# Kernel optimization log

Measured on AMD Instinct MI355X. Metric: run time of the kernel, lower is better.

Reference implementation:

```python
import jax, jax.numpy as jnp
import numpy as np

HEADS = 8
DIM_HEAD = 64
SCALE = DIM_HEAD ** -0.5


def setup_inputs() -> dict:
    key = jax.random.key(0)
    k1, k2, k3, k4 = jax.random.split(key, 4)
    b, dim, l = 4, 512, 2048
    hidden = HEADS * DIM_HEAD  # 512
    x = jax.random.normal(k1, (b, dim, l), dtype=jnp.float32)
    w_qkv = jax.random.normal(k2, (3 * hidden, dim), dtype=jnp.float32) * (dim ** -0.5)
    w_out = jax.random.normal(k3, (dim, hidden), dtype=jnp.float32) * (hidden ** -0.5)
    b_out = jax.random.normal(k4, (dim,), dtype=jnp.float32) * 0.01
    return {"x": x, "w_qkv": w_qkv, "w_out": w_out, "b_out": b_out}


def reference(x, w_qkv, w_out, b_out):
    b, c, l = x.shape
    h, d = HEADS, DIM_HEAD
    # 1x1 Conv1d == channel matmul: [3*hidden, c] x [b, c, l] -> [b, 3*hidden, l]
    qkv = jnp.einsum('oc,bcl->bol', w_qkv, x)
    q, k, v = jnp.split(qkv, 3, axis=1)
    # 'b (h d) l -> b h d l'
    q = q.reshape(b, h, d, l) * SCALE
    k = k.reshape(b, h, d, l)
    v = v.reshape(b, h, d, l)
    sim = jnp.einsum('bhdi,bhdj->bhij', q, k)          # [b, h, l, l]
    attn = jax.nn.softmax(sim, axis=-1)
    out = jnp.einsum('bhij,bhdj->bhid', attn, v)       # [b, h, l, d]
    # 'b h l d -> b (h d) l'
    out = out.transpose(0, 1, 3, 2).reshape(b, h * d, l)
    return jnp.einsum('oc,bcl->bol', w_out, out) + b_out[None, :, None]
```

## Files before the change

### kernel.cpp

```cpp
#include <hip/hip_runtime.h>

#define L_SEQ 2048
#define KDIM  512

typedef __attribute__((ext_vector_type(8))) short short8v;
typedef __attribute__((ext_vector_type(4))) float f32x4;

static __device__ __forceinline__ short f2b(float f) {
    union { float f; unsigned u; } v; v.f = f;
    unsigned r = v.u + 0x7fffu + ((v.u >> 16) & 1u);
    return (short)(r >> 16);
}

static __device__ __forceinline__ float fast_exp2(float x) {
#if __has_builtin(__builtin_amdgcn_exp2f)
    return __builtin_amdgcn_exp2f(x);
#else
    return exp2f(x);
#endif
}

__global__ __launch_bounds__(256) void conv_w(
    const float* __restrict__ wq, const float* __restrict__ wo,
    short* __restrict__ wqb, short* __restrict__ wob)
{
    const int i = blockIdx.x * 256 + threadIdx.x;
    const int NQ = 1536 * 512 / 4;
    float4 v;
    if (i < NQ) v = ((const float4*)wq)[i];
    else        v = ((const float4*)wo)[i - NQ];
    short4 s;
    s.x = f2b(v.x); s.y = f2b(v.y); s.z = f2b(v.z); s.w = f2b(v.w);
    if (i < NQ) ((short4*)wqb)[i] = s;
    else        ((short4*)wob)[i - NQ] = s;
}

__global__ __launch_bounds__(256) void transpose_x(
    const float* __restrict__ x, short* __restrict__ xT)
{
    const int b  = blockIdx.z;
    const int c0 = blockIdx.y * 64;
    const int l0 = blockIdx.x * 64;
    __shared__ __align__(16) float T[64 * 72];
    const int t = threadIdx.x;

#pragma unroll
    for (int j = 0; j < 4; ++j) {
        const int idx = j * 256 + t;
        const int row = idx >> 4, c4 = idx & 15;
        const float4 v = *(const float4*)&x[((size_t)b * KDIM + c0 + row) * L_SEQ + l0 + c4 * 4];
        *(float4*)&T[row * 72 + c4 * 4] = v;
    }
    __syncthreads();

#pragma unroll
    for (int j = 0; j < 2; ++j) {
        const int idx = j * 256 + t;
        const int l = idx >> 3, ch = idx & 7;
        short8v s;
#pragma unroll
        for (int e = 0; e < 8; ++e)
            s[e] = f2b(T[(ch * 8 + e) * 72 + l]);
        *(short8v*)&xT[((size_t)b * L_SEQ + l0 + l) * KDIM + c0 + ch * 8] = s;
    }
}

template<int EPI>
__global__ __launch_bounds__(256) void gemm_bt(
    const short* __restrict__ Ag, const short* __restrict__ Bbase,
    const float* __restrict__ bias,
    short* __restrict__ Qws, short* __restrict__ Kws, short* __restrict__ Vws,
    float* __restrict__ Cout)
{
    const int bz = blockIdx.z;
    const int o0 = blockIdx.y * 128;
    const int l0 = blockIdx.x * 128;
    const short* Bg = Bbase + (size_t)bz * L_SEQ * KDIM;

    __shared__ __align__(16) char smem[2 * 128 * 72 * 2];
    short* sA = (short*)smem;
    short* sB = (short*)(smem + 128 * 72 * 2);

    const int t    = threadIdx.x;
    const int w    = t >> 6;
    const int lane = t & 63;
    const int quad = lane >> 4;
    const int l16  = lane & 15;
    const int wo   = (w & 1) * 64;
    const int wl   = (w >> 1) * 64;

    f32x4 acc[4][4];
#pragma unroll
    for (int i = 0; i < 4; ++i)
#pragma unroll
        for (int n = 0; n < 4; ++n) acc[i][n] = (f32x4){0,0,0,0};

    for (int k0 = 0; k0 < KDIM; k0 += 64) {
#pragma unroll
        for (int j = 0; j < 4; ++j) {
            const int idx = j * 256 + t;
            const int r = idx >> 3, c = idx & 7;
            *(float4*)&sA[r * 72 + c * 8] =
                *(const float4*)&Ag[(size_t)(o0 + r) * KDIM + k0 + c * 8];
            *(float4*)&sB[r * 72 + c * 8] =
                *(const float4*)&Bg[(size_t)(l0 + r) * KDIM + k0 + c * 8];
        }
        __syncthreads();

#pragma unroll
        for (int ks = 0; ks < 2; ++ks) {
            short8v af[4], bf[4];
#pragma unroll
            for (int i = 0; i < 4; ++i)
                af[i] = *(const short8v*)&sA[(wo + i * 16 + l16) * 72 + ks * 32 + quad * 8];
#pragma unroll
            for (int n = 0; n < 4; ++n)
                bf[n] = *(const short8v*)&sB[(wl + n * 16 + l16) * 72 + ks * 32 + quad * 8];
#pragma unroll
            for (int i = 0; i < 4; ++i)
#pragma unroll
                for (int n = 0; n < 4; ++n)
                    acc[i][n] = __builtin_amdgcn_mfma_f32_16x16x32_bf16(af[i], bf[n], acc[i][n], 0, 0, 0);
        }
        __syncthreads();
    }

    if (EPI == 0) {
        const int type  = o0 >> 9;
        const int local = o0 & 511;
        const int bh0   = bz * 8 + (local >> 6);
        const float sc  = (type == 0) ? 0.18033688011112042f : 1.0f;
        short* T = sA;

        if (type == 2) {
#pragma unroll
            for (int i = 0; i < 4; ++i)
#pragma unroll
                for (int n = 0; n < 4; ++n)
#pragma unroll
                    for (int r = 0; r < 4; ++r)
                        T[(wo + i * 16 + quad * 4 + r) * 136 + wl + n * 16 + l16] =
                            f2b(acc[i][n][r]);
            __syncthreads();
#pragma unroll
            for (int p = 0; p < 8; ++p) {
                const int idx = p * 256 + t;
                const int o = idx >> 4, c = idx & 15;
                const float4 v = *(const float4*)&T[o * 136 + c * 8];
                short* dst = Vws + ((size_t)(bh0 + (o >> 6)) * 64 + (o & 63)) * L_SEQ + l0 + c * 8;
                *(float4*)dst = v;
            }
        } else {
#pragma unroll
            for (int i = 0; i < 4; ++i)
#pragma unroll
                for (int n = 0; n < 4; ++n) {
                    short4 s;
                    s.x = f2b(acc[i][n][0] * sc);
                    s.y = f2b(acc[i][n][1] * sc);
                    s.z = f2b(acc[i][n][2] * sc);
                    s.w = f2b(acc[i][n][3] * sc);
                    *(short4*)&T[(wl + n * 16 + l16) * 136 + wo + i * 16 + quad * 4] = s;
                }
            __syncthreads();
            short* base = (type == 0) ? Qws : Kws;
#pragma unroll
            for (int p = 0; p < 8; ++p) {
                const int idx = p * 256 + t;
                const int l = idx >> 4, c = idx & 15;
                const float4 v = *(const float4*)&T[l * 136 + c * 8];
                short* dst = base + ((size_t)(bh0 + (c >> 3)) * L_SEQ + l0 + l) * 64 + (c & 7) * 8;
                *(float4*)dst = v;
            }
        }
    } else {
        float* Cb = Cout + (size_t)bz * KDIM * L_SEQ;
#pragma unroll
        for (int i = 0; i < 4; ++i) {
            const int o = o0 + wo + i * 16 + quad * 4;
            float bv[4];
#pragma unroll
            for (int r = 0; r < 4; ++r) bv[r] = bias[o + r];
#pragma unroll
            for (int n = 0; n < 4; ++n) {
                const int l = l0 + wl + n * 16 + l16;
#pragma unroll
                for (int r = 0; r < 4; ++r)
                    Cb[(size_t)(o + r) * L_SEQ + l] = acc[i][n][r] + bv[r];
            }
        }
    }
}

__global__ __launch_bounds__(256) void attn_mfma(
    const short* __restrict__ Qws, const short* __restrict__ Kws,
    const short* __restrict__ Vws, short* __restrict__ ao)
{
    const int b  = blockIdx.z;
    const int h  = blockIdx.y;
    const int i0 = blockIdx.x * 128;
    const int bh = b * 8 + h;

    __shared__ __align__(16) char smem[36864];
    short* Kld = (short*)smem;
    short* Vld = (short*)(smem + 9216);
    short* Pld = (short*)(smem + 18432);
    float* Old = (float*)smem;

    const int t    = threadIdx.x;
    const int w    = t >> 6;
    const int lane = t & 63;
    const int quad = lane >> 4;
    const int l16  = lane & 15;

    const short* Qb = Qws + (size_t)bh * L_SEQ * 64;
    const short* Kb = Kws + (size_t)bh * L_SEQ * 64;
    const short* Vb = Vws + (size_t)bh * 64 * L_SEQ;

    short8v qa[2][2];
#pragma unroll
    for (int hh = 0; hh < 2; ++hh) {
        const short* qrow = Qb + (size_t)(i0 + w * 32 + hh * 16 + l16) * 64 + quad * 8;
        qa[hh][0] = *(const short8v*)qrow;
        qa[hh][1] = *(const short8v*)(qrow + 32);
    }

    f32x4 oacc[2][4];
#pragma unroll
    for (int hh = 0; hh < 2; ++hh)
#pragma unroll
        for (int n = 0; n < 4; ++n) oacc[hh][n] = (f32x4){0,0,0,0};
    float rsum[2][4] = {{0,0,0,0},{0,0,0,0}};
    short* Pw = Pld + w * 32 * 72;

    for (int j0 = 0; j0 < L_SEQ; j0 += 64) {
        {
            const int r = t >> 2, c = t & 3;
            const float4 k0 = *(const float4*)(Kb + (size_t)(j0 + r) * 64 + c * 16);
            const float4 k1 = *(const float4*)(Kb + (size_t)(j0 + r) * 64 + c * 16 + 8);
            const float4 v0 = *(const float4*)(Vb + (size_t)r * L_SEQ + j0 + c * 16);
            const float4 v1 = *(const float4*)(Vb + (size_t)r * L_SEQ + j0 + c * 16 + 8);
            *(float4*)&Kld[r * 72 + c * 16]     = k0;
            *(float4*)&Kld[r * 72 + c * 16 + 8] = k1;
            *(float4*)&Vld[r * 72 + c * 16]     = v0;
            *(float4*)&Vld[r * 72 + c * 16 + 8] = v1;
        }
        __syncthreads();

        f32x4 sacc[2][4];
#pragma unroll
        for (int hh = 0; hh < 2; ++hh)
#pragma unroll
            for (int n = 0; n < 4; ++n) sacc[hh][n] = (f32x4){0,0,0,0};
#pragma unroll
        for (int n = 0; n < 4; ++n) {
            short8v kf0 = *(const short8v*)&Kld[(n * 16 + l16) * 72 + quad * 8];
            short8v kf1 = *(const short8v*)&Kld[(n * 16 + l16) * 72 + 32 + quad * 8];
#pragma unroll
            for (int hh = 0; hh < 2; ++hh) {
                sacc[hh][n] = __builtin_amdgcn_mfma_f32_16x16x32_bf16(qa[hh][0], kf0, sacc[hh][n], 0, 0, 0);
                sacc[hh][n] = __builtin_amdgcn_mfma_f32_16x16x32_bf16(qa[hh][1], kf1, sacc[hh][n], 0, 0, 0);
            }
        }

#pragma unroll
        for (int hh = 0; hh < 2; ++hh)
#pragma unroll
            for (int n = 0; n < 4; ++n)
#pragma unroll
                for (int r = 0; r < 4; ++r) {
                    const float p = fast_exp2(sacc[hh][n][r]);
                    rsum[hh][r] += p;
                    Pw[(hh * 16 + quad * 4 + r) * 72 + n * 16 + l16] = f2b(p);
                }

        short8v pa[2][2];
#pragma unroll
        for (int hh = 0; hh < 2; ++hh) {
            pa[hh][0] = *(const short8v*)&Pw[(hh * 16 + l16) * 72 + quad * 8];
            pa[hh][1] = *(const short8v*)&Pw[(hh * 16 + l16) * 72 + 32 + quad * 8];
        }
#pragma unroll
        for (int n = 0; n < 4; ++n) {
            short8v vf0 = *(const short8v*)&Vld[(n * 16 + l16) * 72 + quad * 8];
            short8v vf1 = *(const short8v*)&Vld[(n * 16 + l16) * 72 + 32 + quad * 8];
#pragma unroll
            for (int hh = 0; hh < 2; ++hh) {
                oacc[hh][n] = __builtin_amdgcn_mfma_f32_16x16x32_bf16(pa[hh][0], vf0, oacc[hh][n], 0, 0, 0);
                oacc[hh][n] = __builtin_amdgcn_mfma_f32_16x16x32_bf16(pa[hh][1], vf1, oacc[hh][n], 0, 0, 0);
            }
        }
        __syncthreads();
    }

#pragma unroll
    for (int hh = 0; hh < 2; ++hh)
#pragma unroll
        for (int r = 0; r < 4; ++r) {
#pragma unroll
            for (int m = 1; m < 16; m <<= 1)
                rsum[hh][r] += __shfl_xor(rsum[hh][r], m, 64);
            rsum[hh][r] = 1.0f / rsum[hh][r];
        }

#pragma unroll
    for (int hh = 0; hh < 2; ++hh)
#pragma unroll
        for (int n = 0; n < 4; ++n)
#pragma unroll
            for (int r = 0; r < 4; ++r)
                Old[(w * 32 + hh * 16 + quad * 4 + r) * 68 + n * 16 + l16] =
                    oacc[hh][n][r] * rsum[hh][r];
    __syncthreads();
#pragma unroll
    for (int p = 0; p < 8; ++p) {
        const int idx = p * 256 + t;
        const int i = idx >> 4, c4 = idx & 15;
        const float4 v = *(const float4*)&Old[i * 68 + c4 * 4];
        short4 s;
        s.x = f2b(v.x); s.y = f2b(v.y); s.z = f2b(v.z); s.w = f2b(v.w);
        *(short4*)&ao[((size_t)b * L_SEQ + i0 + i) * KDIM + h * 64 + c4 * 4] = s;
    }
}

extern "C" void kernel_launch(void* const* d_in, const int* in_sizes, int n_in,
                              void* d_out, int out_size, void* d_ws, size_t ws_size,
                              hipStream_t stream)
{
    const float* x     = (const float*)d_in[0];
    const float* w_qkv = (const float*)d_in[1];
    const float* w_out = (const float*)d_in[2];
    const float* b_out = (const float*)d_in[3];
    float* out = (float*)d_out;

    char* ws = (char*)d_ws;
    short* xT    = (short*)ws;                      ws += (size_t)4 * L_SEQ * KDIM * 2;
    short* wq_bf = (short*)ws;                      ws += (size_t)1536 * 512 * 2;
    short* wo_bf = (short*)ws;                      ws += (size_t)512 * 512 * 2;
    short* Qws   = (short*)ws;                      ws += (size_t)32 * L_SEQ * 64 * 2;
    short* Kws   = (short*)ws;                      ws += (size_t)32 * L_SEQ * 64 * 2;
    short* Vws   = (short*)ws;                      ws += (size_t)32 * L_SEQ * 64 * 2;
    short* ao    = (short*)ws;

    dim3 blk(256);
    conv_w     <<<dim3(1024), blk, 0, stream>>>(w_qkv, w_out, wq_bf, wo_bf);
    transpose_x<<<dim3(32, 8, 4), blk, 0, stream>>>(x, xT);
    gemm_bt<0> <<<dim3(16, 12, 4), blk, 0, stream>>>(wq_bf, xT, nullptr, Qws, Kws, Vws, nullptr);
    attn_mfma  <<<dim3(16, 8, 4), blk, 0, stream>>>(Qws, Kws, Vws, ao);
    gemm_bt<1> <<<dim3(16, 4, 4), blk, 0, stream>>>(wo_bf, ao, b_out, nullptr, nullptr, nullptr, out);
}
```

Before: 179.3 us.

## Double-buffer K/V in attention, use direct global-to-LDS loads in GEMMs

The attention kernel now keeps two K/V tiles in shared memory and prefetches the next tile into registers while computing on the current one, which removes one barrier per iteration and hides load latency. The GEMM kernels load tiles with global_load_lds straight into unpadded LDS instead of going through registers. The output-projection GEMM uses 64-row tiles, doubling its grid for better occupancy. Risks are larger LDS use in attention (fewer resident blocks) and bank conflicts from the unpadded 64-wide GEMM tiles.

Result: slower. 183.6 us (+2.4%).

```diff
diff --git a/kernel.cpp b/kernel.cpp
--- a/kernel.cpp
+++ b/kernel.cpp
@@ -18,6 +18,13 @@
 #else
     return exp2f(x);
 #endif
+}
+
+static __device__ __forceinline__ void gl2lds16(const short* g, short* l) {
+    __builtin_amdgcn_global_load_lds(
+        (const __attribute__((address_space(1))) unsigned*)g,
+        (__attribute__((address_space(3))) unsigned*)l,
+        16, 0, 0);
 }
 
 __global__ __launch_bounds__(256) void conv_w(
@@ -72,52 +79,65 @@
     short* __restrict__ Qws, short* __restrict__ Kws, short* __restrict__ Vws,
     float* __restrict__ Cout)
 {
+    constexpr int TO   = (EPI == 0) ? 128 : 64;
+    constexpr int WO   = TO / 2;
+    constexpr int NI   = WO / 16;
+    constexpr int CA   = TO * 64 * 2 / 1024;
+    constexpr int CB   = 16;
+    constexpr int CPW  = (CA + CB) / 4;
+    constexpr int SMEM = (EPI == 0) ? 34816 : 24576;
+
     const int bz = blockIdx.z;
-    const int o0 = blockIdx.y * 128;
+    const int o0 = blockIdx.y * TO;
     const int l0 = blockIdx.x * 128;
     const short* Bg = Bbase + (size_t)bz * L_SEQ * KDIM;
 
-    __shared__ __align__(16) char smem[2 * 128 * 72 * 2];
+    __shared__ __align__(16) char smem[SMEM];
     short* sA = (short*)smem;
-    short* sB = (short*)(smem + 128 * 72 * 2);
+    short* sB = (short*)(smem + TO * 64 * 2);
 
     const int t    = threadIdx.x;
     const int w    = t >> 6;
     const int lane = t & 63;
     const int quad = lane >> 4;
     const int l16  = lane & 15;
-    const int wo   = (w & 1) * 64;
+    const int wo   = (w & 1) * WO;
     const int wl   = (w >> 1) * 64;
 
-    f32x4 acc[4][4];
-#pragma unroll
-    for (int i = 0; i < 4; ++i)
+    f32x4 acc[NI][4];
+#pragma unroll
+    for (int i = 0; i < NI; ++i)
 #pragma unroll
         for (int n = 0; n < 4; ++n) acc[i][n] = (f32x4){0,0,0,0};
 
+    const int lrow = lane >> 3;
+    const int lcol = (lane & 7) * 8;
+
     for (int k0 = 0; k0 < KDIM; k0 += 64) {
 #pragma unroll
-        for (int j = 0; j < 4; ++j) {
-            const int idx = j * 256 + t;
-            const int r = idx >> 3, c = idx & 7;
-            *(float4*)&sA[r * 72 + c * 8] =
-                *(const float4*)&Ag[(size_t)(o0 + r) * KDIM + k0 + c * 8];
-            *(float4*)&sB[r * 72 + c * 8] =
-                *(const float4*)&Bg[(size_t)(l0 + r) * KDIM + k0 + c * 8];
+        for (int p = 0; p < CPW; ++p) {
+            const int cid = w * CPW + p;
+            if (cid < CA) {
+                const int row = cid * 8 + lrow;
+                gl2lds16(Ag + (size_t)(o0 + row) * KDIM + k0 + lcol, sA + cid * 512);
+            } else {
+                const int row = (cid - CA) * 8 + lrow;
+                gl2lds16(Bg + (size_t)(l0 + row) * KDIM + k0 + lcol, sB + (cid - CA) * 512);
+            }
         }
         __syncthreads();
 
 #pragma unroll
         for (int ks = 0; ks < 2; ++ks) {
-            short8v af[4], bf[4];
-#pragma unroll
-            for (int i = 0; i < 4; ++i)
-                af[i] = *(const short8v*)&sA[(wo + i * 16 + l16) * 72 + ks * 32 + quad * 8];
+            short8v af[NI], bf[4];
+#pragma unroll
+            for (int i = 0; i < NI; ++i)
+                af[i] = *(const short8v*)&sA[(wo + i * 16 + l16) * 64 + ks * 32 + quad * 8];
 #pragma unroll
             for (int n = 0; n < 4; ++n)
-                bf[n] = *(const short8v*)&sB[(wl + n * 16 + l16) * 72 + ks * 32 + quad * 8];
-#pragma unroll
-            for (int i = 0; i < 4; ++i)
+                bf[n] = *(const short8v*)&sB[(wl + n * 16 + l16) * 64 + ks * 32 + quad * 8];
+#pragma unroll
+            for (int i = 0; i < NI; ++i)
 #pragma unroll
                 for (int n = 0; n < 4; ++n)
                     acc[i][n] = __builtin_amdgcn_mfma_f32_16x16x32_bf16(af[i], bf[n], acc[i][n], 0, 0, 0);
@@ -130,11 +150,11 @@
         const int local = o0 & 511;
         const int bh0   = bz * 8 + (local >> 6);
         const float sc  = (type == 0) ? 0.18033688011112042f : 1.0f;
-        short* T = sA;
+        short* T = (short*)smem;
 
         if (type == 2) {
 #pragma unroll
-            for (int i = 0; i < 4; ++i)
+            for (int i = 0; i < NI; ++i)
 #pragma unroll
                 for (int n = 0; n < 4; ++n)
 #pragma unroll
@@ -152,7 +172,7 @@
             }
         } else {
 #pragma unroll
-            for (int i = 0; i < 4; ++i)
+            for (int i = 0; i < NI; ++i)
 #pragma unroll
                 for (int n = 0; n < 4; ++n) {
                     short4 s;
@@ -176,7 +196,7 @@
     } else {
         float* Cb = Cout + (size_t)bz * KDIM * L_SEQ;
 #pragma unroll
-        for (int i = 0; i < 4; ++i) {
+        for (int i = 0; i < NI; ++i) {
             const int o = o0 + wo + i * 16 + quad * 4;
             float bv[4];
 #pragma unroll
@@ -201,10 +221,8 @@
     const int i0 = blockIdx.x * 128;
     const int bh = b * 8 + h;
 
-    __shared__ __align__(16) char smem[36864];
-    short* Kld = (short*)smem;
-    short* Vld = (short*)(smem + 9216);
-    short* Pld = (short*)(smem + 18432);
+    __shared__ __align__(16) char smem[55296];
+    short* Pld = (short*)(smem + 36864);
     float* Old = (float*)smem;
 
     const int t    = threadIdx.x;
@@ -233,19 +251,36 @@
     float rsum[2][4] = {{0,0,0,0},{0,0,0,0}};
     short* Pw = Pld + w * 32 * 72;
 
+    const int r = t >> 2, c = t & 3;
+    float4 ka, kc, va, vc;
+
+    {
+        short* K0 = (short*)smem;
+        short* V0 = (short*)(smem + 9216);
+        ka = *(const float4*)(Kb + (size_t)r * 64 + c * 16);
+        kc = *(const float4*)(Kb + (size_t)r * 64 + c * 16 + 8);
+        va = *(const float4*)(Vb + (size_t)r * L_SEQ + c * 16);
+        vc = *(const float4*)(Vb + (size_t)r * L_SEQ + c * 16 + 8);
+        *(float4*)&K0[r * 72 + c * 16]     = ka;
+        *(float4*)&K0[r * 72 + c * 16 + 8] = kc;
+        *(float4*)&V0[r * 72 + c * 16]     = va;
+        *(float4*)&V0[r * 72 + c * 16 + 8] = vc;
+    }
+
+    int cur = 0;
     for (int j0 = 0; j0 < L_SEQ; j0 += 64) {
-        {
-            const int r = t >> 2, c = t & 3;
-            const float4 k0 = *(const float4*)(Kb + (size_t)(j0 + r) * 64 + c * 16);
-            const float4 k1 = *(const float4*)(Kb + (size_t)(j0 + r) * 64 + c * 16 + 8);
-            const float4 v0 = *(const float4*)(Vb + (size_t)r * L_SEQ + j0 + c * 16);
-            const float4 v1 = *(const float4*)(Vb + (size_t)r * L_SEQ + j0 + c * 16 + 8);
-            *(float4*)&Kld[r * 72 + c * 16]     = k0;
-            *(float4*)&Kld[r * 72 + c * 16 + 8] = k1;
-            *(float4*)&Vld[r * 72 + c * 16]     = v0;
-            *(float4*)&Vld[r * 72 + c * 16 + 8] = v1;
-        }
         __syncthreads();
+        const short* Kld = (const short*)(smem + cur * 18432);
+        const short* Vld = (const short*)(smem + cur * 18432 + 9216);
+        const bool pf = (j0 + 64 < L_SEQ);
+
+        if (pf) {
+            const int jn = j0 + 64;
+            ka = *(const float4*)(Kb + (size_t)(jn + r) * 64 + c * 16);
+            kc = *(const float4*)(Kb + (size_t)(jn + r) * 64 + c * 16 + 8);
+            va = *(const float4*)(Vb + (size_t)r * L_SEQ + jn + c * 16);
+            vc = *(const float4*)(Vb + (size_t)r * L_SEQ + jn + c * 16 + 8);
+        }
 
         f32x4 sacc[2][4];
 #pragma unroll
@@ -268,10 +303,10 @@
 #pragma unroll
             for (int n = 0; n < 4; ++n)
 #pragma unroll
-                for (int r = 0; r < 4; ++r) {
-                    const float p = fast_exp2(sacc[hh][n][r]);
-                    rsum[hh][r] += p;
-                    Pw[(hh * 16 + quad * 4 + r) * 72 + n * 16 + l16] = f2b(p);
+                for (int rr = 0; rr < 4; ++rr) {
+                    const float p = fast_exp2(sacc[hh][n][rr]);
+                    rsum[hh][rr] += p;
+                    Pw[(hh * 16 + quad * 4 + rr) * 72 + n * 16 + l16] = f2b(p);
                 }
 
         short8v pa[2][2];
@@ -290,27 +325,37 @@
                 oacc[hh][n] = __builtin_amdgcn_mfma_f32_16x16x32_bf16(pa[hh][1], vf1, oacc[hh][n], 0, 0, 0);
             }
         }
-        __syncthreads();
+
+        if (pf) {
+            short* Kn = (short*)(smem + (cur ^ 1) * 18432);
+            short* Vn = (short*)(smem + (cur ^ 1) * 18432 + 9216);
+            *(float4*)&Kn[r * 72 + c * 16]     = ka;
+            *(float4*)&Kn[r * 72 + c * 16 + 8] = kc;
+            *(float4*)&Vn[r * 72 + c * 16]     = va;
+            *(float4*)&Vn[r * 72 + c * 16 + 8] = vc;
+        }
+        cur ^= 1;
     }
 
 #pragma unroll
     for (int hh = 0; hh < 2; ++hh)
 #pragma unroll
-        for (int r = 0; r < 4; ++r) {
+        for (int rr = 0; rr < 4; ++rr) {
 #pragma unroll
             for (int m = 1; m < 16; m <<= 1)
-                rsum[hh][r] += __shfl_xor(rsum[hh][r], m, 64);
-            rsum[hh][r] = 1.0f / rsum[hh][r];
-        }
-
+                rsum[hh][rr] += __shfl_xor(rsum[hh][rr], m, 64);
+            rsum[hh][rr] = 1.0f / rsum[hh][rr];
+        }
+
+    __syncthreads();
 #pragma unroll
     for (int hh = 0; hh < 2; ++hh)
 #pragma unroll
         for (int n = 0; n < 4; ++n)
 #pragma unroll
-            for (int r = 0; r < 4; ++r)
-                Old[(w * 32 + hh * 16 + quad * 4 + r) * 68 + n * 16 + l16] =
-                    oacc[hh][n][r] * rsum[hh][r];
+            for (int rr = 0; rr < 4; ++rr)
+                Old[(w * 32 + hh * 16 + quad * 4 + rr) * 68 + n * 16 + l16] =
+                    oacc[hh][n][rr] * rsum[hh][rr];
     __syncthreads();
 #pragma unroll
     for (int p = 0; p < 8; ++p) {
@@ -347,5 +392,5 @@
     transpose_x<<<dim3(32, 8, 4), blk, 0, stream>>>(x, xT);
     gemm_bt<0> <<<dim3(16, 12, 4), blk, 0, stream>>>(wq_bf, xT, nullptr, Qws, Kws, Vws, nullptr);
     attn_mfma  <<<dim3(16, 8, 4), blk, 0, stream>>>(Qws, Kws, Vws, ao);
-    gemm_bt<1> <<<dim3(16, 4, 4), blk, 0, stream>>>(wo_bf, ao, b_out, nullptr, nullptr, nullptr, out);
-}
+    gemm_bt<1> <<<dim3(16, 8, 4), blk, 0, stream>>>(wo_bf, ao, b_out, nullptr, nullptr, nullptr, out);
+}
```
